# Kernel optimization log

Measured on AMD Instinct MI355X. Metric: run time of the kernel, lower is better.

## Reference

```python
import jax, jax.numpy as jnp
import numpy as np

B, N, D, NH = 16, 512, 4096, 16
DK = D // NH  # 256; note N must equal 2*DK for the bias broadcast to be valid


def setup_inputs() -> dict:
    key = jax.random.key(0)
    ks = jax.random.split(key, 7)
    s = 1.0 / np.sqrt(D).astype(np.float32)
    return {
        "x": jax.random.normal(ks[0], (B, N, D), dtype=jnp.float32),
        "Augementation_embedding": jax.random.normal(ks[1], (B, N, D), dtype=jnp.float32),
        "Wq": jax.random.normal(ks[2], (D, D), dtype=jnp.float32) * s,
        "Wk": jax.random.normal(ks[3], (D, D), dtype=jnp.float32) * s,
        "Wv": jax.random.normal(ks[4], (D, D), dtype=jnp.float32) * s,
        "Wp": jax.random.normal(ks[5], (2 * D, D), dtype=jnp.float32) * s,
        "bp": jax.random.normal(ks[6], (2 * D,), dtype=jnp.float32) * 0.01,
    }


def reference(x, Augementation_embedding, Wq, Wk, Wv, Wp, bp):
    b, n, d = x.shape
    nh, dk = NH, DK
    scale = 1.0 / np.sqrt(dk)
    # torch nn.Linear computes x @ W.T
    q = (x @ Wq.T).reshape(b, n, nh, dk).transpose(0, 2, 1, 3)  # (b,nh,n,dk)
    k = (x @ Wk.T).reshape(b, n, nh, dk).transpose(0, 2, 1, 3)
    v = (x @ Wv.T).reshape(b, n, nh, dk).transpose(0, 2, 1, 3)
    # additive learned bias: (b,nh,n,2*dk) == (b,nh,n,n) since n == 2*dk
    ep = (Augementation_embedding @ Wp.T + bp).reshape(b, n, nh, 2 * dk).transpose(0, 2, 1, 3)
    dist = jnp.einsum("bhqd,bhkd->bhqk", q, k) * scale + ep  # (b,nh,n,n)
    dist = jax.nn.softmax(dist, axis=-1)
    att = jnp.einsum("bhqk,bhkd->bhqd", dist, v)  # (b,nh,n,dk)
    return att.transpose(0, 2, 1, 3).reshape(b, n, d)
```

## Files before the change

### kernel.cpp

```cpp
#include <hip/hip_runtime.h>
#include <hip/hip_bf16.h>

typedef __attribute__((ext_vector_type(4))) float f32x4;
typedef __attribute__((ext_vector_type(8))) short s16x8;
typedef __attribute__((ext_vector_type(4))) short s16x4;
typedef __attribute__((ext_vector_type(8))) unsigned short u16x8;
typedef __attribute__((ext_vector_type(4))) unsigned short u16x4;
typedef __attribute__((ext_vector_type(4))) float fv4;

#define DEV static __device__ __forceinline__

DEV unsigned short f2bf(float f) {
  union { float f; unsigned u; } v; v.f = f;
  return (unsigned short)((v.u + 0x7fffu + ((v.u >> 16) & 1u)) >> 16);
}
DEV float bf2f(unsigned short u) {
  union { unsigned u; float f; } v; v.u = ((unsigned)u) << 16; return v.f;
}

typedef const __attribute__((address_space(1))) void* gas_t;
typedef __attribute__((address_space(3))) void* las_t;
DEV void load_lds16(const void* g, void* l) {
  __builtin_amdgcn_global_load_lds((gas_t)g, (las_t)l, 16, 0, 0);
}

__global__ __launch_bounds__(256) void cvt_kernel(const float* __restrict__ in,
                                                  unsigned short* __restrict__ out,
                                                  int n4) {
  int i = blockIdx.x * 256 + threadIdx.x;
  int stride = gridDim.x * 256;
  for (; i < n4; i += stride) {
    fv4 v = *(const fv4*)(in + (size_t)i * 4);
    u16x4 o;
    o[0] = f2bf(v[0]); o[1] = f2bf(v[1]); o[2] = f2bf(v[2]); o[3] = f2bf(v[3]);
    *(u16x4*)(out + (size_t)i * 4) = o;
  }
}

template<int EPI>
__global__ __launch_bounds__(512, 2) void gemm256(const unsigned short* __restrict__ A,
                                                  const unsigned short* __restrict__ B,
                                                  unsigned short* __restrict__ C,
                                                  const float* __restrict__ bias,
                                                  int N, int K, int nbx_sh) {
  __shared__ unsigned short lds[4][2][8192];
  const int t = threadIdx.x;
  const int lane = t & 63;
  const int w = t >> 6;
  const int wr = w >> 2;
  const int wc = w & 3;
  const int r0 = lane & 15;
  const int g = lane >> 4;

  const int nwg = gridDim.x;
  const int swz = (blockIdx.x & 7) * (nwg >> 3) + (blockIdx.x >> 3);
  const int by = swz >> nbx_sh;
  const int bx = swz & ((1 << nbx_sh) - 1);
  const long brow = (long)by * 256;
  const long bcol = (long)bx * 256;

  const int srow = t >> 2;
  const int scol = ((t & 3) ^ ((t >> 3) & 3)) * 8;
  const unsigned short* As = A + (brow + srow) * (long)K + scol;
  const unsigned short* Bs = B + (bcol + srow) * (long)K + scol;
  const int d0 = t * 8;

#define STAGE(kt, bufi)                                                 \
  do {                                                                  \
    const long k0_ = (long)(kt) << 5;                                   \
    load_lds16(As + k0_,                 &lds[bufi][0][d0]);            \
    load_lds16(As + 128 * (long)K + k0_, &lds[bufi][0][d0 + 4096]);     \
    load_lds16(Bs + k0_,                 &lds[bufi][1][d0]);            \
    load_lds16(Bs + 128 * (long)K + k0_, &lds[bufi][1][d0 + 4096]);     \
  } while (0)

  f32x4 acc[8][4] = {};
  const int NT = K >> 5;

  STAGE(0, 0); STAGE(1, 1); STAGE(2, 2);
  asm volatile("s_waitcnt vmcnt(8)" ::: "memory");
  __builtin_amdgcn_s_barrier();
  __builtin_amdgcn_sched_barrier(0);

  const int cswz = (g ^ ((r0 >> 1) & 3)) * 8;
  const int arow = wr * 128 + r0;
  const int brw = wc * 64 + r0;

  for (int kt = 0; kt < NT; ++kt) {
    const unsigned short* lA = &lds[kt & 3][0][0];
    const unsigned short* lB = &lds[kt & 3][1][0];
    if (kt + 3 < NT) STAGE(kt + 3, (kt + 3) & 3);
    s16x8 av[8], bv[4];
#pragma unroll
    for (int m = 0; m < 8; ++m)
      av[m] = *(const s16x8*)&lA[(arow + m * 16) * 32 + cswz];
#pragma unroll
    for (int n = 0; n < 4; ++n)
      bv[n] = *(const s16x8*)&lB[(brw + n * 16) * 32 + cswz];
    __builtin_amdgcn_s_setprio(1);
#pragma unroll
    for (int m = 0; m < 8; ++m)
#pragma unroll
      for (int n = 0; n < 4; ++n)
        acc[m][n] = __builtin_amdgcn_mfma_f32_16x16x32_bf16(av[m], bv[n], acc[m][n], 0, 0, 0);
    __builtin_amdgcn_s_setprio(0);
    const int rem = NT - 1 - kt;
    if (rem >= 3)      asm volatile("s_waitcnt vmcnt(8)" ::: "memory");
    else if (rem == 2) asm volatile("s_waitcnt vmcnt(4)" ::: "memory");
    else if (rem == 1) asm volatile("s_waitcnt vmcnt(0)" ::: "memory");
    __builtin_amdgcn_s_barrier();
    __builtin_amdgcn_sched_barrier(0);
  }
#undef STAGE

  const int g4 = g * 4;
#pragma unroll
  for (int m = 0; m < 8; ++m) {
#pragma unroll
    for (int n = 0; n < 4; ++n) {
      f32x4 v = acc[m][n];
      long col = bcol + wc * 64 + n * 16 + r0;
#pragma unroll
      for (int r = 0; r < 4; ++r) {
        long row = brow + wr * 128 + m * 16 + g4 + r;
        float val = v[r];
        if (EPI == 1) val += bias[col];
        if (EPI == 2) {
          long addr = ((col >> 9) << 21) + (row << 9) + (col & 511);
          C[addr] = f2bf(val);
        } else {
          C[row * (long)N + col] = f2bf(val);
        }
      }
    }
  }
}

__global__ __launch_bounds__(512, 2) void attn_kernel(const unsigned short* __restrict__ Q,
                                                      const unsigned short* __restrict__ K,
                                                      const unsigned short* __restrict__ V,
                                                      const unsigned short* __restrict__ EP,
                                                      float* __restrict__ out) {
  __shared__ unsigned short lds[256 * 136];
  const int t = threadIdx.x;
  const int lane = t & 63;
  const int w = t >> 6;
  const int bid = blockIdx.x;
  const int qt = bid & 3;
  const int h = (bid >> 2) & 15;
  const int b = bid >> 6;
  const int r0 = lane & 15;
  const int g = lane >> 4;

  const int qrow = qt * 128 + w * 16;

  s16x8 qf[8];
  {
    const unsigned short* qp = Q + ((size_t)(b * 512 + qrow + r0)) * 4096 + h * 256 + g * 8;
#pragma unroll
    for (int s = 0; s < 8; ++s) qf[s] = *(const s16x8*)(qp + s * 32);
  }

  f32x4 st[32];
#pragma unroll
  for (int f = 0; f < 32; ++f) st[f] = f32x4{0.f, 0.f, 0.f, 0.f};

#pragma unroll
  for (int kc = 0; kc < 4; ++kc) {
    {
      const unsigned short* kp = K + ((size_t)(b * 512 + kc * 128)) * 4096 + h * 256;
#pragma unroll
      for (int u = 0; u < 8; ++u) {
        int fidx = u * 4096 + t * 8;
        int row = fidx >> 8, c = fidx & 255;
        u16x8 v = *(const u16x8*)(kp + (size_t)row * 4096 + c);
        *(u16x8*)&lds[row * 264 + c] = v;
      }
    }
    __syncthreads();
#pragma unroll
    for (int mf = 0; mf < 8; ++mf) {
      const unsigned short* lk = &lds[(mf * 16 + r0) * 264 + g * 8];
#pragma unroll
      for (int s = 0; s < 8; ++s) {
        s16x8 af = *(const s16x8*)(lk + s * 32);
        st[kc * 8 + mf] = __builtin_amdgcn_mfma_f32_16x16x32_bf16(af, qf[s], st[kc * 8 + mf], 0, 0, 0);
      }
    }
    __syncthreads();
  }

  {
    const unsigned short* ep = EP + ((size_t)(b * 512 + qrow + r0)) * 8192 + h * 512 + g * 4;
#pragma unroll
    for (int f = 0; f < 32; ++f) {
      u16x4 e = *(const u16x4*)(ep + f * 16);
#pragma unroll
      for (int r = 0; r < 4; ++r)
        st[f][r] = st[f][r] * 0.0625f + bf2f(e[r]);
    }
  }

  float mx = -1e30f;
#pragma unroll
  for (int f = 0; f < 32; ++f)
    mx = fmaxf(mx, fmaxf(fmaxf(st[f][0], st[f][1]), fmaxf(st[f][2], st[f][3])));
  mx = fmaxf(mx, __shfl_xor(mx, 16, 64));
  mx = fmaxf(mx, __shfl_xor(mx, 32, 64));
  float sum = 0.f;
#pragma unroll
  for (int f = 0; f < 32; ++f) {
#pragma unroll
    for (int r = 0; r < 4; ++r) {
      float e = __expf(st[f][r] - mx);
      st[f][r] = e;
      sum += e;
    }
  }
  sum += __shfl_xor(sum, 16, 64);
  sum += __shfl_xor(sum, 32, 64);
  const float rinv = 1.0f / sum;

  s16x8 pb[16];
#pragma unroll
  for (int p = 0; p < 16; ++p) {
    s16x8 v;
#pragma unroll
    for (int j = 0; j < 4; ++j) {
      v[j] = (short)f2bf(st[2 * p][j] * rinv);
      v[j + 4] = (short)f2bf(st[2 * p + 1][j] * rinv);
    }
    pb[p] = v;
  }

  f32x4 acc2[16];
#pragma unroll
  for (int d = 0; d < 16; ++d) acc2[d] = f32x4{0.f, 0.f, 0.f, 0.f};

#pragma unroll
  for (int kc = 0; kc < 4; ++kc) {
    {
      const unsigned short* vp = V + ((size_t)(b * 16 + h)) * 131072 + kc * 128;
#pragma unroll
      for (int u = 0; u < 8; ++u) {
        int fidx = u * 4096 + t * 8;
        int row = fidx >> 7, c = fidx & 127;
        u16x8 vv = *(const u16x8*)(vp + (size_t)row * 512 + c);
        *(u16x8*)&lds[row * 136 + c] = vv;
      }
    }
    __syncthreads();
#pragma unroll
    for (int d = 0; d < 16; ++d) {
      const unsigned short* lv = &lds[(d * 16 + r0) * 136 + g * 4];
#pragma unroll
      for (int p = 0; p < 4; ++p) {
        s16x4 a0 = *(const s16x4*)(lv + p * 32);
        s16x4 a1 = *(const s16x4*)(lv + p * 32 + 16);
        s16x8 av;
        av[0] = a0[0]; av[1] = a0[1]; av[2] = a0[2]; av[3] = a0[3];
        av[4] = a1[0]; av[5] = a1[1]; av[6] = a1[2]; av[7] = a1[3];
        acc2[d] = __builtin_amdgcn_mfma_f32_16x16x32_bf16(av, pb[kc * 4 + p], acc2[d], 0, 0, 0);
      }
    }
    __syncthreads();
  }

  {
    float* op = out + ((size_t)(b * 512 + qrow + r0)) * 4096 + h * 256 + g * 4;
#pragma unroll
    for (int d = 0; d < 16; ++d)
      *(fv4*)(op + d * 16) = acc2[d];
  }
}

extern "C" void kernel_launch(void* const* d_in, const int* in_sizes, int n_in,
                              void* d_out, int out_size, void* d_ws, size_t ws_size,
                              hipStream_t stream) {
  const float* x   = (const float*)d_in[0];
  const float* aug = (const float*)d_in[1];
  const float* wq  = (const float*)d_in[2];
  const float* wk  = (const float*)d_in[3];
  const float* wv  = (const float*)d_in[4];
  const float* wp  = (const float*)d_in[5];
  const float* bp  = (const float*)d_in[6];
  float* out = (float*)d_out;

  const size_t OFF_XA = 0;
  const size_t OFF_WQ = 67108864;
  const size_t OFF_WK = OFF_WQ + 33554432;
  const size_t OFF_WV = OFF_WK + 33554432;
  const size_t OFF_Q  = OFF_WQ + 100663296;
  const size_t OFF_K  = OFF_Q + 67108864;
  const size_t OFF_VT = OFF_K + 67108864;
  const size_t OFF_EP = OFF_VT + 67108864;
  const size_t NEED   = OFF_EP + 134217728;
  if (ws_size < NEED) return;

  char* ws = (char*)d_ws;
  unsigned short* x_bf   = (unsigned short*)(ws + OFF_XA);
  unsigned short* aug_bf = (unsigned short*)(ws + OFF_XA);
  unsigned short* wq_bf  = (unsigned short*)(ws + OFF_WQ);
  unsigned short* wk_bf  = (unsigned short*)(ws + OFF_WK);
  unsigned short* wv_bf  = (unsigned short*)(ws + OFF_WV);
  unsigned short* wp_bf  = (unsigned short*)(ws + OFF_WQ);
  unsigned short* q_bf   = (unsigned short*)(ws + OFF_Q);
  unsigned short* k_bf   = (unsigned short*)(ws + OFF_K);
  unsigned short* vt_bf  = (unsigned short*)(ws + OFF_VT);
  unsigned short* ep_bf  = (unsigned short*)(ws + OFF_EP);

  cvt_kernel<<<2048, 256, 0, stream>>>(x, x_bf, 33554432 / 4);
  cvt_kernel<<<2048, 256, 0, stream>>>(wq, wq_bf, 16777216 / 4);
  cvt_kernel<<<2048, 256, 0, stream>>>(wk, wk_bf, 16777216 / 4);
  cvt_kernel<<<2048, 256, 0, stream>>>(wv, wv_bf, 16777216 / 4);

  gemm256<0><<<512, 512, 0, stream>>>(x_bf, wq_bf, q_bf, nullptr, 4096, 4096, 4);
  gemm256<0><<<512, 512, 0, stream>>>(x_bf, wk_bf, k_bf, nullptr, 4096, 4096, 4);
  gemm256<2><<<512, 512, 0, stream>>>(wv_bf, x_bf, vt_bf, nullptr, 8192, 4096, 5);

  cvt_kernel<<<2048, 256, 0, stream>>>(aug, aug_bf, 33554432 / 4);
  cvt_kernel<<<2048, 256, 0, stream>>>(wp, wp_bf, 33554432 / 4);
  gemm256<1><<<1024, 512, 0, stream>>>(aug_bf, wp_bf, ep_bf, bp, 8192, 4096, 5);

  attn_kernel<<<1024, 512, 0, stream>>>(q_bf, k_bf, vt_bf, ep_bf, out);
}
```

Before: 1.696 ms.

## Restructure GEMM main loop into 8-wave ping-pong phases with K=64 double buffering

Replaces the 4-stage K=32 LDS ring with a double-buffered K=64 tile split into two 32-wide sub-slices. Each iteration runs four phases, each doing half the M rows. Every phase issues one chunk of the next tile's global-to-LDS loads, then a barrier, then a block of MFMAs. Launch bounds drop to one workgroup per CU, so the interleaving of loads, LDS reads and MFMAs within a workgroup has to provide the latency hiding. The cost is more barriers and tighter waitcnt bookkeeping.

```diff
diff --git a/kernel.cpp b/kernel.cpp
--- a/kernel.cpp
+++ b/kernel.cpp
@@ -38,12 +38,12 @@
 }
 
 template<int EPI>
-__global__ __launch_bounds__(512, 2) void gemm256(const unsigned short* __restrict__ A,
+__global__ __launch_bounds__(512, 1) void gemm256(const unsigned short* __restrict__ A,
                                                   const unsigned short* __restrict__ B,
                                                   unsigned short* __restrict__ C,
                                                   const float* __restrict__ bias,
                                                   int N, int K, int nbx_sh) {
-  __shared__ unsigned short lds[4][2][8192];
+  __shared__ unsigned short lds[2][2][2][8192];
   const int t = threadIdx.x;
   const int lane = t & 63;
   const int w = t >> 6;
@@ -63,55 +63,69 @@
   const int scol = ((t & 3) ^ ((t >> 3) & 3)) * 8;
   const unsigned short* As = A + (brow + srow) * (long)K + scol;
   const unsigned short* Bs = B + (bcol + srow) * (long)K + scol;
-  const int d0 = t * 8;
-
-#define STAGE(kt, bufi)                                                 \
-  do {                                                                  \
-    const long k0_ = (long)(kt) << 5;                                   \
-    load_lds16(As + k0_,                 &lds[bufi][0][d0]);            \
-    load_lds16(As + 128 * (long)K + k0_, &lds[bufi][0][d0 + 4096]);     \
-    load_lds16(Bs + k0_,                 &lds[bufi][1][d0]);            \
-    load_lds16(Bs + 128 * (long)K + k0_, &lds[bufi][1][d0 + 4096]);     \
+  const int dst = t * 8;
+
+#define STG(buf, op, ks, kt, Ptr)                                         \
+  do {                                                                    \
+    const long c0_ = ((long)(kt) << 6) + ((ks) << 5);                     \
+    load_lds16(Ptr + c0_,                 &lds[buf][op][ks][dst]);        \
+    load_lds16(Ptr + 128 * (long)K + c0_, &lds[buf][op][ks][4096 + dst]); \
   } while (0)
 
   f32x4 acc[8][4] = {};
-  const int NT = K >> 5;
-
-  STAGE(0, 0); STAGE(1, 1); STAGE(2, 2);
-  asm volatile("s_waitcnt vmcnt(8)" ::: "memory");
+  const int NT = K >> 6;
+
+  STG(0, 0, 0, 0, As); STG(0, 1, 0, 0, Bs);
+  STG(0, 0, 1, 0, As); STG(0, 1, 1, 0, Bs);
+  asm volatile("s_waitcnt vmcnt(4)" ::: "memory");
   __builtin_amdgcn_s_barrier();
-  __builtin_amdgcn_sched_barrier(0);
 
   const int cswz = (g ^ ((r0 >> 1) & 3)) * 8;
   const int arow = wr * 128 + r0;
   const int brw = wc * 64 + r0;
 
+#define PHASE(cb, ks, mq, STMT, WAIT)                                          \
+  do {                                                                         \
+    s16x8 av[4];                                                               \
+    _Pragma("unroll")                                                          \
+    for (int m = 0; m < 4; ++m)                                                \
+      av[m] = *(const s16x8*)&lds[cb][0][ks][(arow + (mq) * 64 + m * 16) * 32 + cswz]; \
+    if ((mq) == 0) {                                                           \
+      _Pragma("unroll")                                                        \
+      for (int n = 0; n < 4; ++n)                                              \
+        bv[n] = *(const s16x8*)&lds[cb][1][ks][(brw + n * 16) * 32 + cswz];    \
+    }                                                                          \
+    STMT;                                                                      \
+    __builtin_amdgcn_s_barrier();                                              \
+    __builtin_amdgcn_s_setprio(1);                                             \
+    _Pragma("unroll")                                                          \
+    for (int m = 0; m < 4; ++m) {                                              \
+      _Pragma("unroll")                                                        \
+      for (int n = 0; n < 4; ++n)                                              \
+        acc[(mq) * 4 + m][n] =                                                 \
+            __builtin_amdgcn_mfma_f32_16x16x32_bf16(av[m], bv[n],              \
+                                                    acc[(mq) * 4 + m][n], 0, 0, 0); \
+    }                                                                          \
+    __builtin_amdgcn_s_setprio(0);                                             \
+    WAIT;                                                                      \
+    __builtin_amdgcn_s_barrier();                                              \
+  } while (0)
+
+#pragma unroll 2
   for (int kt = 0; kt < NT; ++kt) {
-    const unsigned short* lA = &lds[kt & 3][0][0];
-    const unsigned short* lB = &lds[kt & 3][1][0];
-    if (kt + 3 < NT) STAGE(kt + 3, (kt + 3) & 3);
-    s16x8 av[8], bv[4];
-#pragma unroll
-    for (int m = 0; m < 8; ++m)
-      av[m] = *(const s16x8*)&lA[(arow + m * 16) * 32 + cswz];
-#pragma unroll
-    for (int n = 0; n < 4; ++n)
-      bv[n] = *(const s16x8*)&lB[(brw + n * 16) * 32 + cswz];
-    __builtin_amdgcn_s_setprio(1);
-#pragma unroll
-    for (int m = 0; m < 8; ++m)
-#pragma unroll
-      for (int n = 0; n < 4; ++n)
-        acc[m][n] = __builtin_amdgcn_mfma_f32_16x16x32_bf16(av[m], bv[n], acc[m][n], 0, 0, 0);
-    __builtin_amdgcn_s_setprio(0);
-    const int rem = NT - 1 - kt;
-    if (rem >= 3)      asm volatile("s_waitcnt vmcnt(8)" ::: "memory");
-    else if (rem == 2) asm volatile("s_waitcnt vmcnt(4)" ::: "memory");
-    else if (rem == 1) asm volatile("s_waitcnt vmcnt(0)" ::: "memory");
-    __builtin_amdgcn_s_barrier();
-    __builtin_amdgcn_sched_barrier(0);
-  }
-#undef STAGE
+    const int cb = kt & 1, nb = cb ^ 1;
+    const bool st = (kt + 1 < NT);
+    s16x8 bv[4];
+    PHASE(cb, 0, 0, if (st) STG(nb, 0, 0, kt + 1, As), );
+    PHASE(cb, 0, 1, if (st) STG(nb, 1, 0, kt + 1, Bs),
+          if (st) { asm volatile("s_waitcnt vmcnt(4)" ::: "memory"); }
+          else    { asm volatile("s_waitcnt vmcnt(0)" ::: "memory"); });
+    PHASE(cb, 1, 0, if (st) STG(nb, 0, 1, kt + 1, As), );
+    PHASE(cb, 1, 1, if (st) STG(nb, 1, 1, kt + 1, Bs),
+          asm volatile("s_waitcnt vmcnt(4)" ::: "memory"));
+  }
+#undef PHASE
+#undef STG
 
   const int g4 = g * 4;
 #pragma unroll
```

After: 1.719 ms. No clear change (+1.3%).

## Replace 256x256 GEMM tile with 128x256 tile, 4 warps, triple buffering

Applied to the files above, without the earlier changes.

The projection GEMMs now use a 128x256 output tile computed by 256 threads (4 waves, each 64x128), with a 3-slot LDS ring prefetching two stages ahead instead of a 4-slot ring three ahead. The XCD-aware block swizzle is dropped in favour of a plain row-major block mapping, and odd blocks sleep briefly at start to stagger memory traffic. Smaller blocks double the grid size and cut LDS per block, which may raise occupancy and tail balance. In exchange each block reuses less data per loaded operand and L2 locality from the swizzle is lost.

```diff
diff --git a/kernel.cpp b/kernel.cpp
--- a/kernel.cpp
+++ b/kernel.cpp
@@ -38,91 +38,99 @@
 }
 
 template<int EPI>
-__global__ __launch_bounds__(512, 2) void gemm256(const unsigned short* __restrict__ A,
+__global__ __launch_bounds__(256, 2) void gemm128(const unsigned short* __restrict__ A,
                                                   const unsigned short* __restrict__ B,
                                                   unsigned short* __restrict__ C,
                                                   const float* __restrict__ bias,
-                                                  int N, int K, int nbx_sh) {
-  __shared__ unsigned short lds[4][2][8192];
+                                                  int N, int K, int bxsh) {
+  __shared__ unsigned short lds[3][12288];
   const int t = threadIdx.x;
   const int lane = t & 63;
   const int w = t >> 6;
-  const int wr = w >> 2;
-  const int wc = w & 3;
+  const int wr = w >> 1;
+  const int wc = w & 1;
   const int r0 = lane & 15;
   const int g = lane >> 4;
 
-  const int nwg = gridDim.x;
-  const int swz = (blockIdx.x & 7) * (nwg >> 3) + (blockIdx.x >> 3);
-  const int by = swz >> nbx_sh;
-  const int bx = swz & ((1 << nbx_sh) - 1);
-  const long brow = (long)by * 256;
+  const int bid = blockIdx.x;
+  const int bx = bid & ((1 << bxsh) - 1);
+  const int by = bid >> bxsh;
+  const long brow = (long)by * 128;
   const long bcol = (long)bx * 256;
 
   const int srow = t >> 2;
   const int scol = ((t & 3) ^ ((t >> 3) & 3)) * 8;
   const unsigned short* As = A + (brow + srow) * (long)K + scol;
   const unsigned short* Bs = B + (bcol + srow) * (long)K + scol;
-  const int d0 = t * 8;
-
-#define STAGE(kt, bufi)                                                 \
-  do {                                                                  \
-    const long k0_ = (long)(kt) << 5;                                   \
-    load_lds16(As + k0_,                 &lds[bufi][0][d0]);            \
-    load_lds16(As + 128 * (long)K + k0_, &lds[bufi][0][d0 + 4096]);     \
-    load_lds16(Bs + k0_,                 &lds[bufi][1][d0]);            \
-    load_lds16(Bs + 128 * (long)K + k0_, &lds[bufi][1][d0 + 4096]);     \
+  const int dst = t * 8;
+
+#define STG(sl, kt)                                                  \
+  do {                                                               \
+    const long c0_ = (long)(kt) << 5;                                \
+    load_lds16(As + c0_,                   &lds[sl][dst]);           \
+    load_lds16(As + 64 * (long)K + c0_,    &lds[sl][2048 + dst]);    \
+    load_lds16(Bs + c0_,                   &lds[sl][4096 + dst]);    \
+    load_lds16(Bs + 64 * (long)K + c0_,    &lds[sl][6144 + dst]);    \
+    load_lds16(Bs + 128 * (long)K + c0_,   &lds[sl][8192 + dst]);    \
+    load_lds16(Bs + 192 * (long)K + c0_,   &lds[sl][10240 + dst]);   \
   } while (0)
-
-  f32x4 acc[8][4] = {};
+#define SBAR __builtin_amdgcn_sched_barrier(0)
+
+  f32x4 acc[4][8] = {};
   const int NT = K >> 5;
 
-  STAGE(0, 0); STAGE(1, 1); STAGE(2, 2);
-  asm volatile("s_waitcnt vmcnt(8)" ::: "memory");
+  const int cswz = (g ^ ((r0 >> 1) & 3)) * 8;
+  const int arow = wr * 64 + r0;
+  const int brw = wc * 128 + r0;
+
+  if (bid & 1) __builtin_amdgcn_s_sleep(8);
+
+  STG(0, 0);
+  STG(1, 1);
+  asm volatile("s_waitcnt vmcnt(6)" ::: "memory");
   __builtin_amdgcn_s_barrier();
-  __builtin_amdgcn_sched_barrier(0);
-
-  const int cswz = (g ^ ((r0 >> 1) & 3)) * 8;
-  const int arow = wr * 128 + r0;
-  const int brw = wc * 64 + r0;
-
+  SBAR;
+
+  int sl = 0;
   for (int kt = 0; kt < NT; ++kt) {
-    const unsigned short* lA = &lds[kt & 3][0][0];
-    const unsigned short* lB = &lds[kt & 3][1][0];
-    if (kt + 3 < NT) STAGE(kt + 3, (kt + 3) & 3);
-    s16x8 av[8], bv[4];
-#pragma unroll
-    for (int m = 0; m < 8; ++m)
-      av[m] = *(const s16x8*)&lA[(arow + m * 16) * 32 + cswz];
-#pragma unroll
-    for (int n = 0; n < 4; ++n)
-      bv[n] = *(const s16x8*)&lB[(brw + n * 16) * 32 + cswz];
+    int sl2 = sl + 2; if (sl2 >= 3) sl2 -= 3;
+    if (kt + 2 < NT) STG(sl2, kt + 2);
+    const unsigned short* Lp = &lds[sl][0];
+    s16x8 AF[4], BF[8];
+#pragma unroll
+    for (int m = 0; m < 4; ++m)
+      AF[m] = *(const s16x8*)&Lp[(arow + m * 16) * 32 + cswz];
+#pragma unroll
+    for (int n = 0; n < 8; ++n)
+      BF[n] = *(const s16x8*)&Lp[4096 + (brw + n * 16) * 32 + cswz];
+    SBAR;
     __builtin_amdgcn_s_setprio(1);
 #pragma unroll
-    for (int m = 0; m < 8; ++m)
-#pragma unroll
-      for (int n = 0; n < 4; ++n)
-        acc[m][n] = __builtin_amdgcn_mfma_f32_16x16x32_bf16(av[m], bv[n], acc[m][n], 0, 0, 0);
+    for (int m = 0; m < 4; ++m)
+#pragma unroll
+      for (int n = 0; n < 8; ++n)
+        acc[m][n] = __builtin_amdgcn_mfma_f32_16x16x32_bf16(AF[m], BF[n], acc[m][n], 0, 0, 0);
     __builtin_amdgcn_s_setprio(0);
-    const int rem = NT - 1 - kt;
-    if (rem >= 3)      asm volatile("s_waitcnt vmcnt(8)" ::: "memory");
-    else if (rem == 2) asm volatile("s_waitcnt vmcnt(4)" ::: "memory");
-    else if (rem == 1) asm volatile("s_waitcnt vmcnt(0)" ::: "memory");
+    SBAR;
+    if (kt + 2 < NT) asm volatile("s_waitcnt vmcnt(6)" ::: "memory");
+    else             asm volatile("s_waitcnt vmcnt(0)" ::: "memory");
     __builtin_amdgcn_s_barrier();
-    __builtin_amdgcn_sched_barrier(0);
-  }
-#undef STAGE
+    SBAR;
+    sl = (sl == 2) ? 0 : sl + 1;
+  }
+#undef SBAR
+#undef STG
 
   const int g4 = g * 4;
 #pragma unroll
-  for (int m = 0; m < 8; ++m) {
-#pragma unroll
-    for (int n = 0; n < 4; ++n) {
+  for (int m = 0; m < 4; ++m) {
+#pragma unroll
+    for (int n = 0; n < 8; ++n) {
       f32x4 v = acc[m][n];
-      long col = bcol + wc * 64 + n * 16 + r0;
+      long col = bcol + wc * 128 + n * 16 + r0;
 #pragma unroll
       for (int r = 0; r < 4; ++r) {
-        long row = brow + wr * 128 + m * 16 + g4 + r;
+        long row = brow + wr * 64 + m * 16 + g4 + r;
         float val = v[r];
         if (EPI == 1) val += bias[col];
         if (EPI == 2) {
@@ -314,13 +322,13 @@
   cvt_kernel<<<2048, 256, 0, stream>>>(wk, wk_bf, 16777216 / 4);
   cvt_kernel<<<2048, 256, 0, stream>>>(wv, wv_bf, 16777216 / 4);
 
-  gemm256<0><<<512, 512, 0, stream>>>(x_bf, wq_bf, q_bf, nullptr, 4096, 4096, 4);
-  gemm256<0><<<512, 512, 0, stream>>>(x_bf, wk_bf, k_bf, nullptr, 4096, 4096, 4);
-  gemm256<2><<<512, 512, 0, stream>>>(wv_bf, x_bf, vt_bf, nullptr, 8192, 4096, 5);
+  gemm128<0><<<1024, 256, 0, stream>>>(x_bf, wq_bf, q_bf, nullptr, 4096, 4096, 4);
+  gemm128<0><<<1024, 256, 0, stream>>>(x_bf, wk_bf, k_bf, nullptr, 4096, 4096, 4);
+  gemm128<2><<<1024, 256, 0, stream>>>(wv_bf, x_bf, vt_bf, nullptr, 8192, 4096, 5);
 
   cvt_kernel<<<2048, 256, 0, stream>>>(aug, aug_bf, 33554432 / 4);
   cvt_kernel<<<2048, 256, 0, stream>>>(wp, wp_bf, 33554432 / 4);
-  gemm256<1><<<1024, 512, 0, stream>>>(aug_bf, wp_bf, ep_bf, bp, 8192, 4096, 5);
+  gemm128<1><<<2048, 256, 0, stream>>>(aug_bf, wp_bf, ep_bf, bp, 8192, 4096, 5);
 
   attn_kernel<<<1024, 512, 0, stream>>>(q_bf, k_bf, vt_bf, ep_bf, out);
 }
```

After: 1.767 ms. +4.2%, slower.
